# Performance work log

Measured on AMD Instinct MI355X. Metric: run time of the kernel, lower is better.

## Reference

```python
import jax, jax.numpy as jnp
import numpy as np

EPS_COS = 1e-8   # torch F.cosine_similarity eps
EPS_LN = 1e-6    # LayerNorm eps from source


def _attn_block(x, spat, roi, W, b, k):
    """MultiHeadedAttention_3 (flag=1) forward.
    x: [B,N,C], spat: [B,N,2], roi: [B,N,N], W: [h, 2C+4], b: [h].
    query[b,i,j]=x[b,j], key[b,i,j]=x[b,i]; ft = cat(query,key,spat_q,spat_k).
    The linear over the concat is split into per-part einsums (same math,
    avoids materializing the [B,N,N,2C+4] tensor).
    Returns attn1 * roi * topk-scatter mask, shape [B,N,N,h] (dims b,i,j,h).
    """
    B, N, C = x.shape
    Wq, Wk = W[:, :C], W[:, C:2 * C]
    Wsq, Wsk = W[:, 2 * C:2 * C + 2], W[:, 2 * C + 2:]
    qt = jnp.einsum('bjc,hc->bjh', x, Wq) + jnp.einsum('bjs,hs->bjh', spat, Wsq)
    kt = jnp.einsum('bic,hc->bih', x, Wk) + jnp.einsum('bis,hs->bih', spat, Wsk)
    logits = qt[:, None, :, :] + kt[:, :, None, :] + b  # [B,i,j,h]
    attn1 = jax.nn.sigmoid(logits)
    # relu(cosine_similarity(query, key, dim=3)) -> [B,i,j] (symmetric)
    xn = x / jnp.maximum(jnp.linalg.norm(x, axis=-1, keepdims=True), EPS_COS)
    scores = jax.nn.relu(jnp.einsum('bic,bjc->bij', xn, xn))
    # torch: atten_mask[:, :, idces, :] = 1.0 with idces [B,N,k,1] sets, for ALL
    # b,i,h, column j to 1 whenever j appears anywhere in idces (global scatter).
    _, idx = jax.lax.top_k(scores, k)  # [B,N,k]
    present = jnp.zeros((N,), x.dtype).at[idx.reshape(-1)].set(1.0)
    return attn1 * roi[:, :, :, None] * present[None, None, :, None]


def _gconv_relu(x, w, bias):
    """Grouped 1x1 Conv1d + ReLU. x: [B,Cin,N], w: [g, Cout/g, Cin/g]."""
    B, Cin, N = x.shape
    g, og, ig = w.shape
    y = jnp.einsum('bgin,goi->bgon', x.reshape(B, g, ig, N), w)
    return jax.nn.relu(y.reshape(B, g * og, N) + bias[None, :, None])


def _forward(input, masks_roi, score_mask, spat, W1, b1, W2, b2,
             cw1, cb1, cw2, cb2, ln_g, ln_b, node_num):
    B, N, C = input.shape
    h = W1.shape[0]
    masks = masks_roi * score_mask[:, None, :]
    f = (score_mask == 0).astype(input.dtype)          # [B,N]
    f_mask = f[:, :, None] * jnp.eye(N, dtype=input.dtype)  # diag_embed

    A1 = (_attn_block(input, spat, masks, W1, b1, node_num)
          + f_mask[:, :, :, None]) / 4.0               # [B,i,j,h]

    out1 = _gconv_relu(jnp.swapaxes(input, 1, 2), cw1, cb1)  # [B,mid,N]
    mid = out1.shape[1]
    # torch: matmul(out1.view(B,h,mid/h,N), A1.permute(0,3,2,1))  ([B,h,j,i])
    out1m = jnp.einsum('bhdj,bijh->bhdi', out1.reshape(B, h, mid // h, N), A1)
    out1 = out1 + out1m.reshape(B, mid, N)

    x2 = jnp.swapaxes(out1, 1, 2)                      # [B,N,mid]
    A2 = (_attn_block(x2, spat, masks, W2, b2, node_num)
          + f_mask[:, :, :, None]) / 4.0

    out2 = _gconv_relu(out1, cw2, cb2)                 # [B,out,N]
    co = out2.shape[1]
    out2m = jnp.einsum('bhdj,bijh->bhdi', out2.reshape(B, h, co // h, N), A2)
    out2m = jnp.swapaxes(out2m.reshape(B, co, N), 1, 2)  # [B,N,out]
    mu = jnp.mean(out2m, axis=-1, keepdims=True)
    var = jnp.mean(jnp.square(out2m - mu), axis=-1, keepdims=True)
    out2m = (out2m - mu) / jnp.sqrt(var + EPS_LN) * ln_g + ln_b
    out2 = out2 + jnp.swapaxes(out2m, 1, 2)
    return jnp.swapaxes(out2, 1, 2)                    # [B,N,out]


def setup_inputs() -> dict:
    key = jax.random.key(0)
    ks = jax.random.split(key, 10)
    B, N, C, MID, OUT, H, G = 8, 1024, 256, 256, 256, 4, 4
    s = 0.05
    return {
        'input': jax.random.normal(ks[0], (B, N, C), jnp.float32),
        'masks_roi': jax.random.randint(ks[1], (B, N, N), 0, 2).astype(jnp.float32),
        'score_mask': jax.random.randint(ks[2], (B, N), 0, 2).astype(jnp.float32),
        'spat': jax.random.uniform(ks[3], (B, N, 2), jnp.float32),
        'W1': s * jax.random.normal(ks[4], (H, 2 * C + 4), jnp.float32),
        'b1': jnp.zeros((H,), jnp.float32),
        'W2': s * jax.random.normal(ks[5], (H, 2 * MID + 4), jnp.float32),
        'b2': jnp.zeros((H,), jnp.float32),
        'cw1': s * jax.random.normal(ks[6], (G, MID // G, C // G), jnp.float32),
        'cb1': jnp.zeros((MID,), jnp.float32),
        'cw2': s * jax.random.normal(ks[7], (G, OUT // G, MID // G), jnp.float32),
        'cb2': jnp.zeros((OUT,), jnp.float32),
        'ln_g': jnp.ones((OUT,), jnp.float32),
        'ln_b': jnp.zeros((OUT,), jnp.float32),
        'node_num': 16,
    }


def reference(input, masks_roi, score_mask, spat, W1, b1, W2, b2,
              cw1, cb1, cw2, cb2, ln_g, ln_b, node_num):
    return _forward(input, masks_roi, score_mask, spat, W1, b1, W2, b2,
                    cw1, cb1, cw2, cb2, ln_g, ln_b, node_num)
```

## Files before the change

kernel.cpp:

```cpp
#include <hip/hip_runtime.h>

constexpr int Bb = 8;
constexpr int Nn = 1024;
constexpr int Cc = 256;
constexpr int Hh = 4;
constexpr int WROW = 2 * Cc + 4;

typedef float fx4 __attribute__((ext_vector_type(4)));
typedef float f32x4 __attribute__((ext_vector_type(4)));
typedef __bf16 bf16x8 __attribute__((ext_vector_type(8)));

#define GLL16(src, dst)                                                      \
  __builtin_amdgcn_global_load_lds(                                          \
      (const __attribute__((address_space(1))) void*)(src),                  \
      (__attribute__((address_space(3))) void*)(dst), 16, 0, 0)

__global__ __launch_bounds__(256) void k_roipack2(const float* __restrict__ roi,
                                                  const float* __restrict__ sm,
                                                  unsigned long long* __restrict__ roib,
                                                  int* __restrict__ cntb) {
  __shared__ short jmapS[1024];
  __shared__ unsigned char m4S[4][256];
  __shared__ int cntS;
  const int t = threadIdx.x, w = t >> 6, l = t & 63;
  const int gid = blockIdx.x * 4 + w;
  const int b = gid >> 10;

  if (w == 0) {
    int base = 0;
#pragma unroll
    for (int jc = 0; jc < 16; ++jc) {
      const int j = jc * 64 + l;
      const bool act = sm[b * Nn + j] != 0.f;
      const unsigned long long m = __ballot(act);
      if (act) jmapS[base + __popcll(m & ((1ull << l) - 1))] = (short)j;
      base += __popcll(m);
    }
    if (l == 0) {
      cntS = base;
      if ((blockIdx.x & 255) == 0) cntb[b] = base;
    }
  }
  {
    const fx4* r4 = (const fx4*)(roi + (size_t)gid * Nn);
#pragma unroll
    for (int k = 0; k < 4; ++k) {
      fx4 v = r4[k * 64 + l];
      unsigned nb = (v[0] != 0.f ? 1u : 0u) | (v[1] != 0.f ? 2u : 0u) |
                    (v[2] != 0.f ? 4u : 0u) | (v[3] != 0.f ? 8u : 0u);
      m4S[w][k * 64 + l] = (unsigned char)nb;
    }
  }
  __syncthreads();
  const int cnt = cntS;
  unsigned long long* orow = roib + (size_t)gid * 16;
#pragma unroll 4
  for (int pc = 0; pc < 16; ++pc) {
    const int idx = pc * 64 + l;
    const bool valid = idx < cnt;
    const int j = valid ? (int)jmapS[idx] : 0;
    const bool bit = valid && ((m4S[w][j >> 2] >> (j & 3)) & 1);
    unsigned long long m = __ballot(bit);
    if (l == 0) orow[pc] = m;
  }
}

__global__ __launch_bounds__(256) void k_gconvq(const float* __restrict__ src,
                                                const float* __restrict__ cw,
                                                const float* __restrict__ cb,
                                                const float* __restrict__ sm,
                                                const float* __restrict__ spat,
                                                const float* __restrict__ W,
                                                const float* __restrict__ bias,
                                                float* __restrict__ out,
                                                __bf16* __restrict__ gsm,
                                                float* __restrict__ qt,
                                                float* __restrict__ kt) {
  __shared__ __align__(16) bf16x8 xsB[32][32];
  __shared__ __align__(16) float WqkS[8][256];
  __shared__ float cbS[256];
  __shared__ float smS[32];
  __shared__ int pcolS[32];
  __shared__ int actS[32];
  const int b = blockIdx.x, tile = blockIdx.y;
  const int n0 = tile * 32;
  const int t = threadIdx.x, w = t >> 6, l = t & 63;

  if (w == 0) {
    const int fullc = n0 >> 6;
    int cbase = 0;
    unsigned long long am = 0;
    for (int jc = 0; jc <= fullc; ++jc) {
      unsigned long long m = __ballot(sm[b * Nn + jc * 64 + l] != 0.f);
      if (jc < fullc) cbase += __popcll(m); else am = m;
    }
    const int lsel = l - (n0 & 63);
    if (lsel >= 0 && lsel < 32) {
      pcolS[lsel] = cbase + __popcll(am & ((1ull << l) - 1));
      actS[lsel] = (int)((am >> l) & 1);
      smS[lsel] = 0.25f * sm[b * Nn + n0 + lsel];
    }
  }
  cbS[t] = cb[t];
  for (int idx = t; idx < 2048; idx += 256) {
    const int row = idx >> 8, c = idx & 255;
    WqkS[row][c] = W[(row >> 1) * WROW + (row & 1) * Cc + c];
  }

  {
    const int n = t >> 3, c0 = (t & 7) * 32;
    const float* srow = src + ((size_t)(b * Nn + n0 + n)) * Cc + c0;
#pragma unroll
    for (int k = 0; k < 4; ++k) {
      fx4 v0 = *(const fx4*)&srow[k * 8];
      fx4 v1 = *(const fx4*)&srow[k * 8 + 4];
      bf16x8 bv;
#pragma unroll
      for (int e = 0; e < 4; ++e) { bv[e] = (__bf16)v0[e]; bv[4 + e] = (__bf16)v1[e]; }
      xsB[n][((c0 >> 3) + k) ^ (n & 7)] = bv;
    }
  }

  const int g = w, dl = l & 15, q = l >> 4;

  bf16x8 a[4][2];
#pragma unroll
  for (int of = 0; of < 4; ++of)
#pragma unroll
    for (int ks = 0; ks < 2; ++ks) {
      const float* cwp = cw + ((size_t)(g * 64 + of * 16 + dl)) * 64 + ks * 32 + q * 8;
      fx4 c0 = *(const fx4*)cwp;
      fx4 c1 = *(const fx4*)(cwp + 4);
#pragma unroll
      for (int e = 0; e < 4; ++e) { a[of][ks][e] = (__bf16)c0[e]; a[of][ks][4 + e] = (__bf16)c1[e]; }
    }
  __syncthreads();

  f32x4 acc[4][2] = {};
#pragma unroll
  for (int nf = 0; nf < 2; ++nf) {
    const int n = nf * 16 + dl;
#pragma unroll
    for (int ks = 0; ks < 2; ++ks) {
      bf16x8 bv = xsB[n][(g * 8 + ks * 4 + q) ^ (n & 7)];
#pragma unroll
      for (int of = 0; of < 4; ++of)
        acc[of][nf] = __builtin_amdgcn_mfma_f32_16x16x32_bf16(a[of][ks], bv, acc[of][nf], 0, 0, 0);
    }
  }
#pragma unroll
  for (int of = 0; of < 4; ++of)
#pragma unroll
    for (int nf = 0; nf < 2; ++nf) {
      const int n = nf * 16 + dl;
      const float smv = smS[n];
      const int act = actS[n];
      const int pc = pcolS[n];
#pragma unroll
      for (int r = 0; r < 4; ++r) {
        const int co = g * 64 + of * 16 + 4 * q + r;
        const float val = fmaxf(acc[of][nf][r] + cbS[co], 0.f);
        const size_t orow = ((size_t)(b * Cc + co)) * Nn;
        out[orow + n0 + n] = val;
        if (act) gsm[orow + pc] = (__bf16)(smv * val);
      }
    }

  {
    const int nl = l & 31, half = l >> 5;
    float qa = 0.f, ka = 0.f;
#pragma unroll
    for (int k = 0; k < 16; ++k) {
      bf16x8 bv = xsB[nl][(half * 16 + k) ^ (nl & 7)];
      const float* wqp = &WqkS[g * 2 + 0][half * 128 + k * 8];
      const float* wkp = &WqkS[g * 2 + 1][half * 128 + k * 8];
#pragma unroll
      for (int e = 0; e < 8; ++e) {
        const float x = (float)bv[e];
        qa = fmaf(x, wqp[e], qa);
        ka = fmaf(x, wkp[e], ka);
      }
    }
    qa += __shfl_xor(qa, 32, 64);
    ka += __shfl_xor(ka, 32, 64);
    if (l < 32) {
      const int n = n0 + nl;
      const float s0 = spat[(b * Nn + n) * 2 + 0];
      const float s1 = spat[(b * Nn + n) * 2 + 1];
      const float* wsp = W + g * WROW + 2 * Cc;
      const float qf = qa + s0 * wsp[0] + s1 * wsp[1] + bias[g];
      const float kf = ka + s0 * wsp[2] + s1 * wsp[3];
      kt[(b * Hh + g) * Nn + n] = kf * -1.44269504f;
      if (actS[nl]) qt[(b * Hh + g) * Nn + pcolS[nl]] = qf * -1.44269504f;
    }
  }
}

template <int MODE>
__global__ __launch_bounds__(512, 4) void k_apply7(const float* __restrict__ g,
                                                   const __bf16* __restrict__ gsm,
                                                   const float* __restrict__ qt,
                                                   const float* __restrict__ kt,
                                                   const unsigned char* __restrict__ roib,
                                                   const float* __restrict__ sm,
                                                   const int* __restrict__ cntb,
                                                   float* __restrict__ out) {
  __shared__ __align__(16) __bf16 Bs[2][3][2][2048];
  __shared__ __align__(16) float qts[1024];
  __shared__ __align__(16) unsigned char rbs[64 * 128];
  const int b = blockIdx.x, it = blockIdx.y, h = blockIdx.z;
  const int t = threadIdx.x, w = t >> 6, l = t & 63;
  const int grp = w >> 2, wq = w & 3;
  const int i0 = it * 64;
  const int dl = l & 15, q = l >> 4, jqf = q * 8;
  const int iA = i0 + wq * 16 + dl;

  const float kvn = kt[(b * Hh + h) * Nn + iA];
  const float* smrow = sm + b * Nn;

  const int cnt = cntb[b];
  const int stepsTot = (cnt + 63) >> 6;
  const int S = (stepsTot + 1) >> 1;
  const int c0 = grp * S;

  const __bf16* gsrc = gsm + ((size_t)(b * Cc + h * 64 + wq * 16 + (l >> 2))) * Nn
                       + c0 * 64 + (l & 3) * 8;
  __bf16* ring = &Bs[grp][0][0][0];
  const int wdst = wq * 512;
  const int rbbase = (wq * 16 + dl) * 128;

  {
    const float2 qv = *(const float2*)&qt[(b * Hh + h) * Nn + t * 2];
    qts[t * 2 + 0] = qv.x;
    qts[t * 2 + 1] = qv.y;
  }
  {
    const int r = t >> 3, c = (t & 7) * 16;
    const char* src = (const char*)roib + ((size_t)(b * Nn + i0 + r)) * 128 + c;
    *(int4*)&rbs[r * 128 + c] = *(const int4*)src;
  }
  GLL16(gsrc, ring + 0 * 4096 + 0 * 2048 + wdst);
  GLL16(gsrc + 32, ring + 0 * 4096 + 1 * 2048 + wdst);
  GLL16(gsrc + 64, ring + 1 * 4096 + 0 * 2048 + wdst);
  GLL16(gsrc + 96, ring + 1 * 4096 + 1 * 2048 + wdst);
  __syncthreads();

  f32x4 acc[4] = {};
  int cur = 0;

  for (int s = 0; s < S; ++s) {
    const int ck = c0 + s;
    const unsigned int rb0 = rbs[rbbase + ck * 8 + q];
    const unsigned int rb1 = rbs[rbbase + ck * 8 + 4 + q];
    bf16x8 af0, af1;
    {
      fx4 qa = *(const fx4*)&qts[ck * 64 + jqf];
      fx4 qb = *(const fx4*)&qts[ck * 64 + jqf + 4];
#pragma unroll
      for (int e = 0; e < 4; ++e) {
        float sg = __builtin_amdgcn_rcpf(1.f + __builtin_amdgcn_exp2f(qa[e] + kvn));
        af0[e] = (__bf16)(((rb0 >> e) & 1) ? sg : 0.f);
      }
#pragma unroll
      for (int e = 0; e < 4; ++e) {
        float sg = __builtin_amdgcn_rcpf(1.f + __builtin_amdgcn_exp2f(qb[e] + kvn));
        af0[4 + e] = (__bf16)(((rb0 >> (4 + e)) & 1) ? sg : 0.f);
      }
      fx4 qc = *(const fx4*)&qts[ck * 64 + 32 + jqf];
      fx4 qd = *(const fx4*)&qts[ck * 64 + 32 + jqf + 4];
#pragma unroll
      for (int e = 0; e < 4; ++e) {
        float sg = __builtin_amdgcn_rcpf(1.f + __builtin_amdgcn_exp2f(qc[e] + kvn));
        af1[e] = (__bf16)(((rb1 >> e) & 1) ? sg : 0.f);
      }
#pragma unroll
      for (int e = 0; e < 4; ++e) {
        float sg = __builtin_amdgcn_rcpf(1.f + __builtin_amdgcn_exp2f(qd[e] + kvn));
        af1[4 + e] = (__bf16)(((rb1 >> (4 + e)) & 1) ? sg : 0.f);
      }
    }
    asm volatile("s_waitcnt vmcnt(2)\n\ts_barrier" ::: "memory");
    __builtin_amdgcn_sched_barrier(0);
    {
      const int nc = s + 2;
      const int off = (nc < S) ? nc * 64 : 0;
      const int pf = (cur == 0) ? 2 : cur - 1;
      GLL16(gsrc + off, ring + pf * 4096 + 0 * 2048 + wdst);
      GLL16(gsrc + off + 32, ring + pf * 4096 + 1 * 2048 + wdst);
    }
    const __bf16* bp = ring + cur * 4096;
#pragma unroll
    for (int nf = 0; nf < 4; ++nf) {
      bf16x8 bv = *(const bf16x8*)(bp + (nf * 16 + dl) * 32 + jqf);
      acc[nf] = __builtin_amdgcn_mfma_f32_16x16x32_bf16(af0, bv, acc[nf], 0, 0, 0);
    }
#pragma unroll
    for (int nf = 0; nf < 4; ++nf) {
      bf16x8 bv = *(const bf16x8*)(bp + 2048 + (nf * 16 + dl) * 32 + jqf);
      acc[nf] = __builtin_amdgcn_mfma_f32_16x16x32_bf16(af1, bv, acc[nf], 0, 0, 0);
    }
    cur = (cur == 2) ? 0 : cur + 1;
  }

  __syncthreads();
  float* accS = (float*)&Bs[0][0][0][0];
  if (grp == 1) {
#pragma unroll
    for (int nf = 0; nf < 4; ++nf)
      *(f32x4*)&accS[((wq * 64 + l) * 4 + nf) * 4] = acc[nf];
  }
  __syncthreads();
  if (grp == 0) {
#pragma unroll
    for (int nf = 0; nf < 4; ++nf)
      acc[nf] += *(const f32x4*)&accS[((wq * 64 + l) * 4 + nf) * 4];

    const int iw = i0 + wq * 16 + (l >> 4) * 4;
    fx4 sv = *(const fx4*)&smrow[iw];
    float fv[4];
#pragma unroll
    for (int r = 0; r < 4; ++r) fv[r] = (sv[r] == 0.f) ? 0.25f : 0.f;
#pragma unroll
    for (int nf = 0; nf < 4; ++nf) {
      const int ch = h * 64 + nf * 16 + dl;
      fx4 gv = *(const fx4*)&g[((size_t)(b * Cc + ch)) * Nn + iw];
#pragma unroll
      for (int r = 0; r < 4; ++r) {
        const float res = (MODE == 0) ? gv[r] * (1.f + fv[r]) + acc[nf][r]
                                      : acc[nf][r] + fv[r] * gv[r];
        out[((size_t)b * Nn + iw + r) * Cc + ch] = res;
      }
    }
  }
}

__global__ __launch_bounds__(256) void k_lnfinal(float* __restrict__ io,
                                                 const float* __restrict__ g2,
                                                 const float* __restrict__ lng,
                                                 const float* __restrict__ lnb) {
  __shared__ float gt[32][258];
  const int b = blockIdx.x, i0 = blockIdx.y * 32;
  const int t = threadIdx.x, w = t >> 6, l = t & 63;
  {
    const int n = t & 31, ch = t >> 5;
#pragma unroll 8
    for (int rr = 0; rr < 32; ++rr) {
      int c = rr * 8 + ch;
      gt[n][c] = g2[((size_t)(b * Cc + c)) * Nn + i0 + n];
    }
  }
  __syncthreads();
  const fx4 lngv = *(const fx4*)&lng[l * 4];
  const fx4 lnbv = *(const fx4*)&lnb[l * 4];
#pragma unroll
  for (int r = 0; r < 8; ++r) {
    const int n = r * 4 + w;
    const size_t base = ((size_t)(b * Nn) + i0 + n) * Cc + l * 4;
    fx4 v = *(const fx4*)&io[base];
    float s = v[0] + v[1] + v[2] + v[3];
    float sq = v[0] * v[0] + v[1] * v[1] + v[2] * v[2] + v[3] * v[3];
#pragma unroll
    for (int off = 32; off; off >>= 1) {
      s += __shfl_xor(s, off, 64);
      sq += __shfl_xor(sq, off, 64);
    }
    const float m = s * (1.f / 256.f);
    const float var = sq * (1.f / 256.f) - m * m;
    const float rstd = rsqrtf(fmaxf(var, 0.f) + 1e-6f);
    fx4 gv = *(const fx4*)&gt[n][l * 4];
    fx4 res;
#pragma unroll
    for (int e = 0; e < 4; ++e)
      res[e] = gv[e] + (v[e] - m) * rstd * lngv[e] + lnbv[e];
    *(fx4*)&io[base] = res;
  }
}

extern "C" void kernel_launch(void* const* d_in, const int* in_sizes, int n_in,
                              void* d_out, int out_size, void* d_ws, size_t ws_size,
                              hipStream_t stream) {
  (void)in_sizes; (void)n_in; (void)out_size; (void)ws_size;
  const float* input = (const float*)d_in[0];
  const float* roi   = (const float*)d_in[1];
  const float* sm    = (const float*)d_in[2];
  const float* spat  = (const float*)d_in[3];
  const float* W1    = (const float*)d_in[4];
  const float* b1    = (const float*)d_in[5];
  const float* W2    = (const float*)d_in[6];
  const float* b2    = (const float*)d_in[7];
  const float* cw1   = (const float*)d_in[8];
  const float* cb1   = (const float*)d_in[9];
  const float* cw2   = (const float*)d_in[10];
  const float* cb2   = (const float*)d_in[11];
  const float* lng   = (const float*)d_in[12];
  const float* lnb   = (const float*)d_in[13];

  float* outf = (float*)d_out;
  char* ws = (char*)d_ws;
  const size_t PLANE = (size_t)Bb * Cc * Nn;
  float* gbuf = (float*)ws;
  __bf16* gsm = (__bf16*)(ws + PLANE * 4);
  unsigned long long* roib =
      (unsigned long long*)(ws + PLANE * 4 + PLANE * 2);
  float* qtb = (float*)((char*)roib + (size_t)Bb * Nn * 128);
  float* ktb = qtb + Bb * Hh * Nn;
  int* cntb = (int*)(ktb + Bb * Hh * Nn);
  float* out1 = outf;

  k_roipack2<<<dim3(2048), 256, 0, stream>>>(roi, sm, roib, cntb);
  k_gconvq<<<dim3(8, 32), 256, 0, stream>>>(input, cw1, cb1, sm, spat, W1, b1,
                                            gbuf, gsm, qtb, ktb);
  k_apply7<0><<<dim3(8, 16, 4), 512, 0, stream>>>(gbuf, gsm, qtb, ktb,
                                                  (const unsigned char*)roib, sm,
                                                  cntb, out1);
  k_gconvq<<<dim3(8, 32), 256, 0, stream>>>(out1, cw2, cb2, sm, spat, W2, b2,
                                            gbuf, gsm, qtb, ktb);
  k_apply7<1><<<dim3(8, 16, 4), 512, 0, stream>>>(gbuf, gsm, qtb, ktb,
                                                  (const unsigned char*)roib, sm,
                                                  cntb, outf);
  k_lnfinal<<<dim3(8, 32), 256, 0, stream>>>(outf, gbuf, lng, lnb);
}
```

Baseline: 74.62 us.

## Fuse final LayerNorm into second apply kernel via last-block atomic counter

Removes the separate LayerNorm kernel. Each (batch, row-tile) now has a counter that the four head blocks of the second apply pass increment atomically. The last block to finish normalizes that 64-row tile in place, adds the conv residual staged through reused shared memory, and writes the result. This saves a kernel launch and a full pass over the output, but adds a memset launch, threadfence and atomic traffic, and a serialized tail done by only one block per tile.

```diff
diff --git a/kernel.cpp b/kernel.cpp
--- a/kernel.cpp
+++ b/kernel.cpp
@@ -204,10 +204,14 @@
                                                    const unsigned char* __restrict__ roib,
                                                    const float* __restrict__ sm,
                                                    const int* __restrict__ cntb,
-                                                   float* __restrict__ out) {
+                                                   float* __restrict__ out,
+                                                   const float* __restrict__ lng,
+                                                   const float* __restrict__ lnb,
+                                                   int* __restrict__ lncnt) {
   __shared__ __align__(16) __bf16 Bs[2][3][2][2048];
   __shared__ __align__(16) float qts[1024];
   __shared__ __align__(16) unsigned char rbs[64 * 128];
+  __shared__ int lastS;
   const int b = blockIdx.x, it = blockIdx.y, h = blockIdx.z;
   const int t = threadIdx.x, w = t >> 6, l = t & 63;
   const int grp = w >> 2, wq = w & 3;
@@ -332,47 +336,57 @@
       }
     }
   }
-}
-
-__global__ __launch_bounds__(256) void k_lnfinal(float* __restrict__ io,
-                                                 const float* __restrict__ g2,
-                                                 const float* __restrict__ lng,
-                                                 const float* __restrict__ lnb) {
-  __shared__ float gt[32][258];
-  const int b = blockIdx.x, i0 = blockIdx.y * 32;
-  const int t = threadIdx.x, w = t >> 6, l = t & 63;
-  {
-    const int n = t & 31, ch = t >> 5;
-#pragma unroll 8
-    for (int rr = 0; rr < 32; ++rr) {
-      int c = rr * 8 + ch;
-      gt[n][c] = g2[((size_t)(b * Cc + c)) * Nn + i0 + n];
-    }
-  }
-  __syncthreads();
-  const fx4 lngv = *(const fx4*)&lng[l * 4];
-  const fx4 lnbv = *(const fx4*)&lnb[l * 4];
-#pragma unroll
-  for (int r = 0; r < 8; ++r) {
-    const int n = r * 4 + w;
-    const size_t base = ((size_t)(b * Nn) + i0 + n) * Cc + l * 4;
-    fx4 v = *(const fx4*)&io[base];
-    float s = v[0] + v[1] + v[2] + v[3];
-    float sq = v[0] * v[0] + v[1] * v[1] + v[2] * v[2] + v[3] * v[3];
-#pragma unroll
-    for (int off = 32; off; off >>= 1) {
-      s += __shfl_xor(s, off, 64);
-      sq += __shfl_xor(sq, off, 64);
-    }
-    const float m = s * (1.f / 256.f);
-    const float var = sq * (1.f / 256.f) - m * m;
-    const float rstd = rsqrtf(fmaxf(var, 0.f) + 1e-6f);
-    fx4 gv = *(const fx4*)&gt[n][l * 4];
-    fx4 res;
-#pragma unroll
-    for (int e = 0; e < 4; ++e)
-      res[e] = gv[e] + (v[e] - m) * rstd * lngv[e] + lnbv[e];
-    *(fx4*)&io[base] = res;
+
+  if (MODE == 1) {
+    __syncthreads();
+    if (t == 0) {
+      __threadfence();
+      const int old = atomicAdd(&lncnt[b * 16 + it], 1);
+      if (old == 3) __threadfence();
+      lastS = (old == 3) ? 1 : 0;
+    }
+    __syncthreads();
+    if (lastS) {
+      float* gt = (float*)&Bs[0][0][0][0];
+      const fx4 lngv = *(const fx4*)&lng[l * 4];
+      const fx4 lnbv = *(const fx4*)&lnb[l * 4];
+#pragma unroll
+      for (int chunk = 0; chunk < 2; ++chunk) {
+        const int ib = i0 + chunk * 32;
+        {
+          const int n = t & 31, ch = t >> 5;
+#pragma unroll 4
+          for (int rr = 0; rr < 16; ++rr) {
+            const int c = rr * 16 + ch;
+            gt[n * 258 + c] = g[((size_t)(b * Cc + c)) * Nn + ib + n];
+          }
+        }
+        __syncthreads();
+#pragma unroll
+        for (int r = 0; r < 4; ++r) {
+          const int n = r * 8 + w;
+          const size_t base = ((size_t)(b * Nn) + ib + n) * Cc + l * 4;
+          fx4 v = *(const fx4*)&out[base];
+          float s = v[0] + v[1] + v[2] + v[3];
+          float sq = v[0] * v[0] + v[1] * v[1] + v[2] * v[2] + v[3] * v[3];
+#pragma unroll
+          for (int off = 32; off; off >>= 1) {
+            s += __shfl_xor(s, off, 64);
+            sq += __shfl_xor(sq, off, 64);
+          }
+          const float m = s * (1.f / 256.f);
+          const float var = sq * (1.f / 256.f) - m * m;
+          const float rstd = rsqrtf(fmaxf(var, 0.f) + 1e-6f);
+          fx4 gv = *(const fx4*)&gt[n * 258 + l * 4];
+          fx4 res;
+#pragma unroll
+          for (int e = 0; e < 4; ++e)
+            res[e] = gv[e] + (v[e] - m) * rstd * lngv[e] + lnbv[e];
+          *(fx4*)&out[base] = res;
+        }
+        __syncthreads();
+      }
+    }
   }
 }
 
@@ -405,18 +419,19 @@
   float* qtb = (float*)((char*)roib + (size_t)Bb * Nn * 128);
   float* ktb = qtb + Bb * Hh * Nn;
   int* cntb = (int*)(ktb + Bb * Hh * Nn);
+  int* lncnt = cntb + 8;
   float* out1 = outf;
 
+  hipMemsetAsync(lncnt, 0, 128 * sizeof(int), stream);
   k_roipack2<<<dim3(2048), 256, 0, stream>>>(roi, sm, roib, cntb);
   k_gconvq<<<dim3(8, 32), 256, 0, stream>>>(input, cw1, cb1, sm, spat, W1, b1,
                                             gbuf, gsm, qtb, ktb);
   k_apply7<0><<<dim3(8, 16, 4), 512, 0, stream>>>(gbuf, gsm, qtb, ktb,
                                                   (const unsigned char*)roib, sm,
-                                                  cntb, out1);
+                                                  cntb, out1, lng, lnb, lncnt);
   k_gconvq<<<dim3(8, 32), 256, 0, stream>>>(out1, cw2, cb2, sm, spat, W2, b2,
                                             gbuf, gsm, qtb, ktb);
   k_apply7<1><<<dim3(8, 16, 4), 512, 0, stream>>>(gbuf, gsm, qtb, ktb,
                                                   (const unsigned char*)roib, sm,
-                                                  cntb, outf);
-  k_lnfinal<<<dim3(8, 32), 256, 0, stream>>>(outf, gbuf, lng, lnb);
+                                                  cntb, outf, lng, lnb, lncnt);
 }
```

Result: slower. 97.94 us (+31.3%).
